# Kernel optimization log

Measured on AMD Instinct MI355X. Metric: run time of the kernel, lower is better.

## Reference

```python
import jax, jax.numpy as jnp
import numpy as np

# static config (matches init_kwargs)
C, NH, WS, H, W, NQ, PS = 384, 12, 8, 56, 56, 64, 8
HD = C // NH
SCALE = HD ** -0.5
EPS = 1e-5
MLP_H = 4 * C


def _rel_pos_index():
    ch, cw = np.meshgrid(np.arange(WS), np.arange(WS), indexing='ij')
    cf = np.stack([ch.ravel(), cw.ravel()])                      # [2, WS*WS]
    rel = cf[:, :, None] - cf[:, None, :]                        # [2, N, N]
    rel = rel.transpose(1, 2, 0)
    rel[:, :, 0] += WS - 1
    rel[:, :, 1] += WS - 1
    rel[:, :, 0] *= 2 * WS - 1
    return jnp.asarray(rel.sum(-1))                              # [N, N] int

REL_IDX = _rel_pos_index()


def _ln(x, g, b):
    mu = x.mean(-1, keepdims=True)
    var = ((x - mu) ** 2).mean(-1, keepdims=True)
    return (x - mu) * jax.lax.rsqrt(var + EPS) * g + b


def setup_inputs() -> dict:
    key = jax.random.key(0)
    ks = jax.random.split(key, 24)
    B = 16
    n = lambda k, shp, s=0.02: jax.random.normal(k, shp, dtype=jnp.float32) * s
    inp = {
        'x': jax.random.normal(ks[0], (B, H * W, C), dtype=jnp.float32),
        'query_tokens': n(ks[1], (1, NQ, C)),
        'kproj_w': n(ks[2], (C, C)), 'kproj_b': jnp.zeros((C,)),
        'kbn_g': jnp.ones((C,)), 'kbn_b': jnp.zeros((C,)),
        'vproj_w': n(ks[3], (C, C)), 'vproj_b': jnp.zeros((C,)),
        'vbn_g': jnp.ones((C,)), 'vbn_b': jnp.zeros((C,)),
        'ck_w': n(ks[4], (C, C)), 'ck_b': jnp.zeros((C,)),
        'cv_w': n(ks[5], (C, C)), 'cv_b': jnp.zeros((C,)),
        'qkv_w': n(ks[6], (C, 3 * C)), 'qkv_b': jnp.zeros((3 * C,)),
        'proj_w': n(ks[7], (C, C)), 'proj_b': jnp.zeros((C,)),
        'rpb_table': n(ks[8], ((2 * WS - 1) ** 2, NH)),
        'norm1_g': jnp.ones((C,)), 'norm1_b': jnp.zeros((C,)),
        'norm2_g': jnp.ones((C,)), 'norm2_b': jnp.zeros((C,)),
        'fc1_w': n(ks[9], (C, MLP_H)), 'fc1_b': jnp.zeros((MLP_H,)),
        'fc2_w': n(ks[10], (MLP_H, C)), 'fc2_b': jnp.zeros((C,)),
    }
    return inp


def _forward(x, query_tokens, kproj_w, kproj_b, kbn_g, kbn_b, vproj_w, vproj_b,
             vbn_g, vbn_b, ck_w, ck_b, cv_w, cv_b, qkv_w, qkv_b, proj_w, proj_b,
             rpb_table, norm1_g, norm1_b, norm2_g, norm2_b, fc1_w, fc1_b, fc2_w, fc2_b):
    B, L, _ = x.shape
    shortcut = x
    xn = _ln(x, norm1_g, norm1_b)                                # [B, L, C]

    # ---- global cross attention (pooled tokens -> learnable queries) ----
    x4 = xn.reshape(B, H, W, C)
    pooled = x4.reshape(B, H // PS, PS, W // PS, PS, C).mean(axis=(2, 4))  # [B,7,7,C]
    pooled = pooled.reshape(B, (H // PS) * (W // PS), C)         # [B, 49, C]
    # conv1x1 + BatchNorm2d (eval mode, default running stats mean=0, var=1)
    bn_scale = 1.0 / jnp.sqrt(1.0 + EPS)
    key = ((pooled @ kproj_w + kproj_b) * bn_scale) * kbn_g + kbn_b
    val = ((pooled @ vproj_w + vproj_b) * bn_scale) * vbn_g + vbn_b

    q = jnp.broadcast_to(query_tokens, (B, NQ, C))
    qh = q.reshape(B, NQ, NH, HD).transpose(0, 2, 1, 3)          # [B,NH,NQ,HD]
    kh = key.reshape(B, -1, NH, HD).transpose(0, 2, 1, 3)
    vh = val.reshape(B, -1, NH, HD).transpose(0, 2, 1, 3)
    attn = jax.nn.softmax(jnp.einsum('bhqd,bhkd->bhqk', qh, kh) * SCALE, axis=-1)
    o = jnp.einsum('bhqk,bhkd->bhqd', attn, vh).transpose(0, 2, 1, 3).reshape(B, NQ, C)
    gk = (o + q) @ ck_w + ck_b                                   # [B, NQ, C]
    gv = (o + q) @ cv_w + cv_b

    # ---- windowed attention with global kv concat ----
    nW = (H // WS) * (W // WS)
    N = WS * WS
    xw = (x4.reshape(B, H // WS, WS, W // WS, WS, C)
             .transpose(0, 1, 3, 2, 4, 5)
             .reshape(B * nW, N, C))                             # [B_, N, C]
    qkv = (xw @ qkv_w + qkv_b).reshape(B * nW, N, 3, NH, HD).transpose(2, 0, 3, 1, 4)
    wq, wk, wv = qkv[0], qkv[1], qkv[2]                          # [B_, NH, N, HD]

    gkh = jnp.broadcast_to(gk.reshape(B, 1, NQ, NH, HD), (B, nW, NQ, NH, HD))
    gkh = gkh.reshape(B * nW, NQ, NH, HD).transpose(0, 2, 1, 3)  # [B_, NH, NQ, HD]
    gvh = jnp.broadcast_to(gv.reshape(B, 1, NQ, NH, HD), (B, nW, NQ, NH, HD))
    gvh = gvh.reshape(B * nW, NQ, NH, HD).transpose(0, 2, 1, 3)
    wk = jnp.concatenate([wk, gkh], axis=2)                      # [B_, NH, N+NQ, HD]
    wv = jnp.concatenate([wv, gvh], axis=2)

    logits = jnp.einsum('bhqd,bhkd->bhqk', wq * SCALE, wk)       # [B_, NH, N, N+NQ]
    rpb = rpb_table[REL_IDX.reshape(-1)].reshape(N, N, NH).transpose(2, 0, 1)  # [NH,N,N]
    logits = logits.at[:, :, :, :N].add(rpb[None])
    wattn = jax.nn.softmax(logits, axis=-1)
    ow = jnp.einsum('bhqk,bhkd->bhqd', wattn, wv).transpose(0, 2, 1, 3).reshape(B * nW, N, C)
    ow = ow @ proj_w + proj_b

    # window reverse
    xr = (ow.reshape(B, H // WS, W // WS, WS, WS, C)
             .transpose(0, 1, 3, 2, 4, 5)
             .reshape(B, H * W, C))

    x = shortcut + xr
    h = jax.nn.gelu(_ln(x, norm2_g, norm2_b) @ fc1_w + fc1_b, approximate=False)
    return x + (h @ fc2_w + fc2_b)


def reference(x, query_tokens, kproj_w, kproj_b, kbn_g, kbn_b, vproj_w, vproj_b,
              vbn_g, vbn_b, ck_w, ck_b, cv_w, cv_b, qkv_w, qkv_b, proj_w, proj_b,
              rpb_table, norm1_g, norm1_b, norm2_g, norm2_b, fc1_w, fc1_b, fc2_w, fc2_b):
    return _forward(x, query_tokens, kproj_w, kproj_b, kbn_g, kbn_b, vproj_w, vproj_b,
                    vbn_g, vbn_b, ck_w, ck_b, cv_w, cv_b, qkv_w, qkv_b, proj_w, proj_b,
                    rpb_table, norm1_g, norm1_b, norm2_g, norm2_b, fc1_w, fc1_b, fc2_w, fc2_b)
```

## Files before the change

### kernel.cpp

```cpp
#include <hip/hip_runtime.h>
#include <math.h>

typedef __attribute__((ext_vector_type(8))) __bf16 bf16x8;
typedef __attribute__((ext_vector_type(4))) float f32x4;
typedef __attribute__((ext_vector_type(8))) unsigned short u16x8;

#define DI __device__ __forceinline__

DI float b2f(unsigned short u) { return __uint_as_float(((unsigned int)u) << 16); }
DI unsigned short f2b(float f) {
    unsigned int x = __float_as_uint(f);
    x += 0x7fffu + ((x >> 16) & 1u);
    return (unsigned short)(x >> 16);
}
DI unsigned short f2b_fast(float f) {
    __bf16 h = (__bf16)f;
    return *(unsigned short*)&h;
}

DI void gl16(const unsigned short* g, unsigned short* l) {
    __builtin_amdgcn_global_load_lds(
        (const __attribute__((address_space(1))) void*)g,
        (__attribute__((address_space(3))) void*)l,
        16, 0, 0);
}

DI float gelu_f(float v) {
    float u = v * (0.7978845608f + 0.0356774081f * v * v);
    u = fminf(fmaxf(u, -15.f), 15.f);
    float e = __expf(2.f * u);
    float th = (e - 1.f) / (e + 1.f);
    return 0.5f * v * (1.f + th);
}

#define SCALE_ATT 0.17677669529663687f
#define BN_SCALE  0.9999950000374997f

__global__ __launch_bounds__(256) void cvt_t_kernel(const float* __restrict__ in,
                                                    unsigned short* __restrict__ out,
                                                    int Kd, int Nd) {
    int i = blockIdx.x * 256 + threadIdx.x;
    if (i < Kd * Nd) {
        int k = i / Nd, n = i % Nd;
        out[(size_t)n * Kd + k] = f2b(in[i]);
    }
}

__global__ __launch_bounds__(64) void ln_kernel(const float* __restrict__ xin,
                                                const float* __restrict__ g,
                                                const float* __restrict__ bsh,
                                                unsigned short* __restrict__ out) {
    int row = blockIdx.x;
    int t = threadIdx.x;
    size_t base = (size_t)row * 384;
    float v[6];
    float s = 0.f;
#pragma unroll
    for (int p = 0; p < 6; ++p) { v[p] = xin[base + t + 64 * p]; s += v[p]; }
#pragma unroll
    for (int off = 32; off > 0; off >>= 1) s += __shfl_xor(s, off);
    float mu = s * (1.f / 384.f);
    float q = 0.f;
#pragma unroll
    for (int p = 0; p < 6; ++p) { float d = v[p] - mu; q += d * d; }
#pragma unroll
    for (int off = 32; off > 0; off >>= 1) q += __shfl_xor(q, off);
    float rstd = rsqrtf(q * (1.f / 384.f) + 1e-5f);
#pragma unroll
    for (int p = 0; p < 6; ++p) {
        int c = t + 64 * p;
        out[base + c] = f2b((v[p] - mu) * rstd * g[c] + bsh[c]);
    }
}

__global__ __launch_bounds__(384) void pool_kernel(const unsigned short* __restrict__ xn,
                                                   float* __restrict__ pooled) {
    int blk = blockIdx.x;
    int b = blk / 49, pp = blk % 49;
    int ph = pp / 7, pw = pp % 7;
    int c = threadIdx.x;
    float s = 0.f;
    for (int i = 0; i < 8; ++i) {
        size_t rb = ((size_t)b * 3136 + (size_t)(ph * 8 + i) * 56 + pw * 8) * 384;
        for (int j = 0; j < 8; ++j) s += b2f(xn[rb + (size_t)j * 384 + c]);
    }
    pooled[(size_t)blk * 384 + c] = s * (1.f / 64.f);
}

__global__ __launch_bounds__(128) void kvproj_kernel(
    const float* __restrict__ pooled,
    const float* __restrict__ kw, const float* __restrict__ kb,
    const float* __restrict__ kg, const float* __restrict__ kbb,
    const float* __restrict__ vw, const float* __restrict__ vb,
    const float* __restrict__ vg, const float* __restrict__ vbb,
    float* __restrict__ keyo, float* __restrict__ valo) {
    __shared__ float row[384];
    int r = blockIdx.x;
    int t = threadIdx.x;
    for (int c = t; c < 384; c += 128) row[c] = pooled[(size_t)r * 384 + c];
    __syncthreads();
#pragma unroll
    for (int p = 0; p < 3; ++p) {
        int c = t + 128 * p;
        float aK = 0.f, aV = 0.f;
        for (int k = 0; k < 384; ++k) {
            float rv = row[k];
            aK += rv * kw[(size_t)k * 384 + c];
            aV += rv * vw[(size_t)k * 384 + c];
        }
        keyo[(size_t)r * 384 + c] = (aK + kb[c]) * BN_SCALE * kg[c] + kbb[c];
        valo[(size_t)r * 384 + c] = (aV + vb[c]) * BN_SCALE * vg[c] + vbb[c];
    }
}

__global__ __launch_bounds__(64) void rpb_expand_kernel(const float* __restrict__ rpbt,
                                                        float* __restrict__ rpb_mat) {
    int h = blockIdx.x >> 6, q = blockIdx.x & 63;
    int k = threadIdx.x;
    int i1 = q >> 3, j1 = q & 7, i2 = k >> 3, j2 = k & 7;
    rpb_mat[((size_t)h * 64 + q) * 64 + k] = rpbt[(size_t)((i1 - i2 + 7) * 15 + (j1 - j2 + 7)) * 12 + h];
}

__global__ __launch_bounds__(64) void cross_attn_kernel(const float* __restrict__ keyg,
                                                        const float* __restrict__ valg,
                                                        const float* __restrict__ qtok,
                                                        float* __restrict__ o) {
    int b = blockIdx.x / 12, h = blockIdx.x % 12;
    __shared__ float kk[49][32];
    __shared__ float vv[49][32];
    int t = threadIdx.x;
    for (int idx = t; idx < 49 * 32; idx += 64) {
        int k = idx >> 5, d = idx & 31;
        size_t gidx = ((size_t)b * 49 + k) * 384 + h * 32 + d;
        kk[k][d] = keyg[gidx];
        vv[k][d] = valg[gidx];
    }
    __syncthreads();
    float q[32];
#pragma unroll
    for (int d = 0; d < 32; ++d) q[d] = qtok[(size_t)t * 384 + h * 32 + d] * SCALE_ATT;
    float lg[49];
    float mx = -1e30f;
#pragma unroll
    for (int k = 0; k < 49; ++k) {
        float s = 0.f;
#pragma unroll
        for (int d = 0; d < 32; ++d) s += q[d] * kk[k][d];
        lg[k] = s;
        mx = fmaxf(mx, s);
    }
    float sum = 0.f;
#pragma unroll
    for (int k = 0; k < 49; ++k) { float e = expf(lg[k] - mx); lg[k] = e; sum += e; }
    float inv = 1.f / sum;
    float od[32];
#pragma unroll
    for (int d = 0; d < 32; ++d) od[d] = 0.f;
#pragma unroll
    for (int k = 0; k < 49; ++k) {
        float wgt = lg[k];
#pragma unroll
        for (int d = 0; d < 32; ++d) od[d] += wgt * vv[k][d];
    }
#pragma unroll
    for (int d = 0; d < 32; ++d) o[((size_t)b * 64 + t) * 384 + h * 32 + d] = od[d] * inv;
}

__global__ __launch_bounds__(128) void gkv_kernel(
    const float* __restrict__ o, const float* __restrict__ qtok,
    const float* __restrict__ ckw, const float* __restrict__ ckb,
    const float* __restrict__ cvw, const float* __restrict__ cvb,
    unsigned short* __restrict__ gk, unsigned short* __restrict__ gv) {
    __shared__ float row[384];
    int r = blockIdx.x;
    int n = r & 63;
    int t = threadIdx.x;
    for (int c = t; c < 384; c += 128)
        row[c] = o[(size_t)r * 384 + c] + qtok[(size_t)n * 384 + c];
    __syncthreads();
#pragma unroll
    for (int p = 0; p < 3; ++p) {
        int c = t + 128 * p;
        float aK = 0.f, aV = 0.f;
        for (int k = 0; k < 384; ++k) {
            float rv = row[k];
            aK += rv * ckw[(size_t)k * 384 + c];
            aV += rv * cvw[(size_t)k * 384 + c];
        }
        gk[(size_t)r * 384 + c] = f2b(aK + ckb[c]);
        gv[(size_t)r * 384 + c] = f2b(aV + cvb[c]);
    }
}

template <int MODE>
__global__ __launch_bounds__(256) void gemm128(const unsigned short* __restrict__ A,
                                               const unsigned short* __restrict__ BT,
                                               const float* __restrict__ bias,
                                               int N, int K,
                                               void* __restrict__ outp,
                                               const void* __restrict__ aux0) {
    __shared__ __align__(16) unsigned short As[2][128 * 32];
    __shared__ __align__(16) unsigned short Bs[2][128 * 32];

    int nwg = gridDim.x * gridDim.y;
    int flat = blockIdx.y * gridDim.x + blockIdx.x;
    int flat2 = (flat & 7) * (nwg >> 3) + (flat >> 3);
    int bn = flat2 % gridDim.x, bm = flat2 / gridDim.x;

    int t = threadIdx.x;
    int w = t >> 6, lane = t & 63;
    int wm = w >> 1, wn = w & 1;
    int lo = lane & 15, g = lane >> 4;

    f32x4 acc[4][4];
#pragma unroll
    for (int i = 0; i < 4; ++i)
#pragma unroll
        for (int j = 0; j < 4; ++j) acc[i][j] = f32x4{0.f, 0.f, 0.f, 0.f};

    int srow = w * 32 + (lane >> 2);
    int schunk = (lane & 3) << 3;
    const unsigned short* Ap0 = A + (size_t)(bm * 128 + srow) * K + schunk;
    const unsigned short* Ap1 = A + (size_t)(bm * 128 + srow + 16) * K + schunk;
    const unsigned short* Bp0 = BT + (size_t)(bn * 128 + srow) * K + schunk;
    const unsigned short* Bp1 = BT + (size_t)(bn * 128 + srow + 16) * K + schunk;
    int d0 = (w * 32) * 32, d1 = (w * 32 + 16) * 32;

#define STAGE(buf, kb)                    \
    do {                                  \
        gl16(Ap0 + (kb), As[buf] + d0);   \
        gl16(Ap1 + (kb), As[buf] + d1);   \
        gl16(Bp0 + (kb), Bs[buf] + d0);   \
        gl16(Bp1 + (kb), Bs[buf] + d1);   \
    } while (0)

#define WAITBAR()                                          \
    do {                                                   \
        asm volatile("s_waitcnt vmcnt(0)" ::: "memory");   \
        __builtin_amdgcn_s_barrier();                      \
    } while (0)

#define COMPUTE(buf)                                                                     \
    do {                                                                                 \
        bf16x8 af[4], bfv[4];                                                            \
        _Pragma("unroll")                                                                \
        for (int m = 0; m < 4; ++m)                                                      \
            af[m] = *(const bf16x8*)(As[buf] + (wm * 64 + m * 16 + lo) * 32 + g * 8);    \
        _Pragma("unroll")                                                                \
        for (int n = 0; n < 4; ++n)                                                      \
            bfv[n] = *(const bf16x8*)(Bs[buf] + (wn * 64 + n * 16 + lo) * 32 + g * 8);   \
        _Pragma("unroll")                                                                \
        for (int m = 0; m < 4; ++m)                                                      \
            _Pragma("unroll")                                                            \
            for (int n = 0; n < 4; ++n)                                                  \
                acc[m][n] = __builtin_amdgcn_mfma_f32_16x16x32_bf16(af[m], bfv[n],       \
                                                                    acc[m][n], 0, 0, 0); \
    } while (0)

    STAGE(0, 0);
    WAITBAR();

    int nt = K >> 5;
    for (int tt = 0; tt < nt; tt += 2) {
        STAGE(1, (tt + 1) * 32);
        COMPUTE(0);
        WAITBAR();
        if (tt + 2 < nt) {
            STAGE(0, (tt + 2) * 32);
            COMPUTE(1);
            WAITBAR();
        } else {
            COMPUTE(1);
        }
    }
#undef STAGE
#undef WAITBAR
#undef COMPUTE

    int r0 = bm * 128 + wm * 64 + g * 4;
    int c0 = bn * 128 + wn * 64 + lo;
#pragma unroll
    for (int m = 0; m < 4; ++m)
#pragma unroll
        for (int n = 0; n < 4; ++n)
#pragma unroll
            for (int j = 0; j < 4; ++j) {
                int r = r0 + m * 16 + j;
                int c = c0 + n * 16;
                float v = acc[m][n][j] + bias[c];
                if (MODE == 0) {
                    ((unsigned short*)outp)[(size_t)r * N + c] = f2b(v);
                } else if (MODE == 1) {
                    int wg = r >> 6, nn = r & 63;
                    int b = wg / 49, win = wg % 49;
                    int wh = win / 7, ww = win % 7;
                    int l = ((wh << 3) + (nn >> 3)) * 56 + (ww << 3) + (nn & 7);
                    size_t idx = ((size_t)b * 3136 + l) * 384 + c;
                    ((float*)outp)[idx] = ((const float*)aux0)[idx] + v;
                } else if (MODE == 2) {
                    ((unsigned short*)outp)[(size_t)r * N + c] = f2b(gelu_f(v));
                } else {
                    float res = ((const float*)aux0)[(size_t)r * 384 + c];
                    ((float*)outp)[(size_t)r * N + c] = v + res;
                }
            }
}

__global__ __launch_bounds__(64, 2) void win_attn_mfma(const unsigned short* __restrict__ qkv,
                                                       const unsigned short* __restrict__ gkb,
                                                       const unsigned short* __restrict__ gvb,
                                                       const float* __restrict__ rpb_mat,
                                                       unsigned short* __restrict__ ow) {
    int blk = blockIdx.x;
    int wg = blk / 12, h = blk % 12;
    int b = wg / 49, win = wg % 49;
    int wh = win / 7, ww = win % 7;
    int lane = threadIdx.x;
    int lo = lane & 15, g = lane >> 4;

    __shared__ __align__(16) unsigned short VT[32 * 136];
    __shared__ __align__(16) unsigned short PL[64 * 40];

    size_t qkvbase = (size_t)b * 3136 * 1152;
    int lbase = ((wh << 3)) * 56 + (ww << 3);

    {
        int n = lane;
        int l = lbase + (n >> 3) * 56 + (n & 7);
        const unsigned short* vp = qkv + qkvbase + (size_t)l * 1152 + 768 + h * 32;
        u16x8 v0 = *(const u16x8*)(vp);
        u16x8 v1 = *(const u16x8*)(vp + 8);
        u16x8 v2 = *(const u16x8*)(vp + 16);
        u16x8 v3 = *(const u16x8*)(vp + 24);
#pragma unroll
        for (int j = 0; j < 8; ++j) {
            VT[(0 + j) * 136 + n]  = v0[j];
            VT[(8 + j) * 136 + n]  = v1[j];
            VT[(16 + j) * 136 + n] = v2[j];
            VT[(24 + j) * 136 + n] = v3[j];
        }
        const unsigned short* gp = gvb + ((size_t)b * 64 + n) * 384 + h * 32;
        v0 = *(const u16x8*)(gp);
        v1 = *(const u16x8*)(gp + 8);
        v2 = *(const u16x8*)(gp + 16);
        v3 = *(const u16x8*)(gp + 24);
#pragma unroll
        for (int j = 0; j < 8; ++j) {
            VT[(0 + j) * 136 + 64 + n]  = v0[j];
            VT[(8 + j) * 136 + 64 + n]  = v1[j];
            VT[(16 + j) * 136 + 64 + n] = v2[j];
            VT[(24 + j) * 136 + 64 + n] = v3[j];
        }
    }

    bf16x8 qf[4];
#pragma unroll
    for (int qt = 0; qt < 4; ++qt) {
        int n = qt * 16 + lo;
        int l = lbase + (n >> 3) * 56 + (n & 7);
        qf[qt] = *(const bf16x8*)(qkv + qkvbase + (size_t)l * 1152 + h * 32 + g * 8);
    }

    f32x4 S[4][8];
#pragma unroll
    for (int qt = 0; qt < 4; ++qt)
#pragma unroll
        for (int t = 0; t < 8; ++t) S[qt][t] = f32x4{0.f, 0.f, 0.f, 0.f};

#pragma unroll
    for (int t = 0; t < 8; ++t) {
        bf16x8 kf;
        if (t < 4) {
            int key = t * 16 + lo;
            int l = lbase + (key >> 3) * 56 + (key & 7);
            kf = *(const bf16x8*)(qkv + qkvbase + (size_t)l * 1152 + 384 + h * 32 + g * 8);
        } else {
            int gkey = (t - 4) * 16 + lo;
            kf = *(const bf16x8*)(gkb + ((size_t)b * 64 + gkey) * 384 + h * 32 + g * 8);
        }
#pragma unroll
        for (int qt = 0; qt < 4; ++qt)
            S[qt][t] = __builtin_amdgcn_mfma_f32_16x16x32_bf16(qf[qt], kf, S[qt][t], 0, 0, 0);
    }

    const float* rb_h = rpb_mat + (size_t)h * 4096;
    float mx[4][4];
#pragma unroll
    for (int qt = 0; qt < 4; ++qt)
#pragma unroll
        for (int j = 0; j < 4; ++j) mx[qt][j] = -1e30f;

#pragma unroll
    for (int qt = 0; qt < 4; ++qt) {
#pragma unroll
        for (int t = 0; t < 8; ++t) {
#pragma unroll
            for (int j = 0; j < 4; ++j) {
                float v = S[qt][t][j] * SCALE_ATT;
                if (t < 4) v += rb_h[(qt * 16 + g * 4 + j) * 64 + t * 16 + lo];
                S[qt][t][j] = v;
                mx[qt][j] = fmaxf(mx[qt][j], v);
            }
        }
    }
#pragma unroll
    for (int qt = 0; qt < 4; ++qt)
#pragma unroll
        for (int j = 0; j < 4; ++j) {
#pragma unroll
            for (int m = 1; m <= 8; m <<= 1)
                mx[qt][j] = fmaxf(mx[qt][j], __shfl_xor(mx[qt][j], m));
        }

    float sm[4][4];
#pragma unroll
    for (int qt = 0; qt < 4; ++qt)
#pragma unroll
        for (int j = 0; j < 4; ++j) sm[qt][j] = 0.f;
#pragma unroll
    for (int qt = 0; qt < 4; ++qt)
#pragma unroll
        for (int t = 0; t < 8; ++t)
#pragma unroll
            for (int j = 0; j < 4; ++j) {
                float p = __expf(S[qt][t][j] - mx[qt][j]);
                S[qt][t][j] = p;
                sm[qt][j] += p;
            }
#pragma unroll
    for (int qt = 0; qt < 4; ++qt)
#pragma unroll
        for (int j = 0; j < 4; ++j) {
#pragma unroll
            for (int m = 1; m <= 8; m <<= 1)
                sm[qt][j] += __shfl_xor(sm[qt][j], m);
        }
    float inv[4][4];
#pragma unroll
    for (int qt = 0; qt < 4; ++qt)
#pragma unroll
        for (int j = 0; j < 4; ++j) inv[qt][j] = 1.f / sm[qt][j];

    f32x4 O[4][2];
#pragma unroll
    for (int qt = 0; qt < 4; ++qt)
#pragma unroll
        for (int dt = 0; dt < 2; ++dt) O[qt][dt] = f32x4{0.f, 0.f, 0.f, 0.f};

#pragma unroll
    for (int c = 0; c < 4; ++c) {
        __syncthreads();
#pragma unroll
        for (int qt = 0; qt < 4; ++qt) {
            int qb = qt * 16 + g * 4;
#pragma unroll
            for (int half = 0; half < 2; ++half) {
                int t = 2 * c + half;
#pragma unroll
                for (int j = 0; j < 4; ++j)
                    PL[(qb + j) * 40 + half * 16 + lo] = f2b_fast(S[qt][t][j]);
            }
        }
        __syncthreads();
#pragma unroll
        for (int qt = 0; qt < 4; ++qt) {
            bf16x8 pa = *(const bf16x8*)(PL + (qt * 16 + lo) * 40 + g * 8);
#pragma unroll
            for (int dt = 0; dt < 2; ++dt) {
                bf16x8 vb = *(const bf16x8*)(VT + (dt * 16 + lo) * 136 + c * 32 + g * 8);
                O[qt][dt] = __builtin_amdgcn_mfma_f32_16x16x32_bf16(pa, vb, O[qt][dt], 0, 0, 0);
            }
        }
    }

#pragma unroll
    for (int qt = 0; qt < 4; ++qt)
#pragma unroll
        for (int dt = 0; dt < 2; ++dt)
#pragma unroll
            for (int j = 0; j < 4; ++j) {
                int q = qt * 16 + g * 4 + j;
                int d = dt * 16 + lo;
                ow[((size_t)wg * 64 + q) * 384 + h * 32 + d] = f2b_fast(O[qt][dt][j] * inv[qt][j]);
            }
}

static const size_t OFF_XN   = 0;
static const size_t OFF_QKV  = 38535168;
static const size_t OFF_OW   = 154140672;
static const size_t OFF_X2   = 192675840;
static const size_t OFF_PL   = 269746176;
static const size_t OFF_KEY  = 270950400;
static const size_t OFF_VAL  = 272154624;
static const size_t OFF_O    = 273358848;
static const size_t OFF_GK   = 274931712;
static const size_t OFF_GV   = 276504576;
static const size_t OFF_QKVW = 278077440;
static const size_t OFF_PRJW = 278962176;
static const size_t OFF_FC1W = 279257088;
static const size_t OFF_FC2W = 280436736;

extern "C" void kernel_launch(void* const* d_in, const int* in_sizes, int n_in,
                              void* d_out, int out_size, void* d_ws, size_t ws_size,
                              hipStream_t stream) {
    const float* x      = (const float*)d_in[0];
    const float* qtok   = (const float*)d_in[1];
    const float* kprojw = (const float*)d_in[2];
    const float* kprojb = (const float*)d_in[3];
    const float* kbng   = (const float*)d_in[4];
    const float* kbnb   = (const float*)d_in[5];
    const float* vprojw = (const float*)d_in[6];
    const float* vprojb = (const float*)d_in[7];
    const float* vbng   = (const float*)d_in[8];
    const float* vbnb   = (const float*)d_in[9];
    const float* ckw    = (const float*)d_in[10];
    const float* ckb    = (const float*)d_in[11];
    const float* cvw    = (const float*)d_in[12];
    const float* cvb    = (const float*)d_in[13];
    const float* qkvw   = (const float*)d_in[14];
    const float* qkvb   = (const float*)d_in[15];
    const float* projw  = (const float*)d_in[16];
    const float* projb  = (const float*)d_in[17];
    const float* rpbt   = (const float*)d_in[18];
    const float* n1g    = (const float*)d_in[19];
    const float* n1b    = (const float*)d_in[20];
    const float* n2g    = (const float*)d_in[21];
    const float* n2b    = (const float*)d_in[22];
    const float* fc1w   = (const float*)d_in[23];
    const float* fc1b   = (const float*)d_in[24];
    const float* fc2w   = (const float*)d_in[25];
    const float* fc2b   = (const float*)d_in[26];

    char* wsb = (char*)d_ws;
    unsigned short* xn     = (unsigned short*)(wsb + OFF_XN);
    unsigned short* qkvbf  = (unsigned short*)(wsb + OFF_QKV);
    unsigned short* owbf   = (unsigned short*)(wsb + OFF_OW);
    float* x2      = (float*)(wsb + OFF_X2);
    float* pooled  = (float*)(wsb + OFF_PL);
    float* rpb_mat = (float*)(wsb + OFF_PL);
    float* keyg    = (float*)(wsb + OFF_KEY);
    float* valg    = (float*)(wsb + OFF_VAL);
    float* obuf    = (float*)(wsb + OFF_O);
    unsigned short* gkb = (unsigned short*)(wsb + OFF_GK);
    unsigned short* gvb = (unsigned short*)(wsb + OFF_GV);
    unsigned short* qkvw_t = (unsigned short*)(wsb + OFF_QKVW);
    unsigned short* prjw_t = (unsigned short*)(wsb + OFF_PRJW);
    unsigned short* fc1w_t = (unsigned short*)(wsb + OFF_FC1W);
    unsigned short* fc2w_t = (unsigned short*)(wsb + OFF_FC2W);
    unsigned short* ln2out = (unsigned short*)(wsb + OFF_XN);
    unsigned short* hbuf   = (unsigned short*)(wsb + OFF_QKV);

    cvt_t_kernel<<<(442368 + 255) / 256, 256, 0, stream>>>(qkvw, qkvw_t, 384, 1152);
    cvt_t_kernel<<<(147456 + 255) / 256, 256, 0, stream>>>(projw, prjw_t, 384, 384);
    cvt_t_kernel<<<(589824 + 255) / 256, 256, 0, stream>>>(fc1w, fc1w_t, 384, 1536);
    cvt_t_kernel<<<(589824 + 255) / 256, 256, 0, stream>>>(fc2w, fc2w_t, 1536, 384);
    ln_kernel<<<50176, 64, 0, stream>>>(x, n1g, n1b, xn);
    pool_kernel<<<784, 384, 0, stream>>>(xn, pooled);
    kvproj_kernel<<<784, 128, 0, stream>>>(pooled, kprojw, kprojb, kbng, kbnb,
                                           vprojw, vprojb, vbng, vbnb, keyg, valg);
    rpb_expand_kernel<<<768, 64, 0, stream>>>(rpbt, rpb_mat);
    cross_attn_kernel<<<192, 64, 0, stream>>>(keyg, valg, qtok, obuf);
    gkv_kernel<<<1024, 128, 0, stream>>>(obuf, qtok, ckw, ckb, cvw, cvb, gkb, gvb);
    gemm128<0><<<dim3(9, 392), 256, 0, stream>>>(xn, qkvw_t, qkvb, 1152, 384, qkvbf, nullptr);
    win_attn_mfma<<<9408, 64, 0, stream>>>(qkvbf, gkb, gvb, rpb_mat, owbf);
    gemm128<1><<<dim3(3, 392), 256, 0, stream>>>(owbf, prjw_t, projb, 384, 384, x2, x);
    ln_kernel<<<50176, 64, 0, stream>>>(x2, n2g, n2b, ln2out);
    gemm128<2><<<dim3(12, 392), 256, 0, stream>>>(ln2out, fc1w_t, fc1b, 1536, 384, hbuf, nullptr);
    gemm128<3><<<dim3(3, 392), 256, 0, stream>>>(hbuf, fc2w_t, fc2b, 384, 1536, (float*)d_out, x2);
}
```

Baseline: 823.3 us.

## Triple-buffer GEMM LDS staging with partial vmcnt waits

The bf16 MFMA GEMM goes from double-buffered to triple-buffered LDS tiles. Each stage now waits with vmcnt(4), so one tile's global-to-LDS loads stay in flight while the current tile is computed, and it uses a single barrier per k-step instead of a full drain. The aim is to hide global load latency better. In exchange, shared memory per block rises to 48KB, and the launch bound now asks for 3 blocks per SM, which may put pressure on registers or LDS. The loop unrolls by 3, so it assumes K/32 is a multiple of 3, which holds for the 384 and 1536 K sizes used.

Measured after the change: 715.6 us. 13.1% less time.

```diff
diff --git a/kernel.cpp b/kernel.cpp
--- a/kernel.cpp
+++ b/kernel.cpp
@@ -193,14 +193,14 @@
 }
 
 template <int MODE>
-__global__ __launch_bounds__(256) void gemm128(const unsigned short* __restrict__ A,
-                                               const unsigned short* __restrict__ BT,
-                                               const float* __restrict__ bias,
-                                               int N, int K,
-                                               void* __restrict__ outp,
-                                               const void* __restrict__ aux0) {
-    __shared__ __align__(16) unsigned short As[2][128 * 32];
-    __shared__ __align__(16) unsigned short Bs[2][128 * 32];
+__global__ __launch_bounds__(256, 3) void gemm128(const unsigned short* __restrict__ A,
+                                                  const unsigned short* __restrict__ BT,
+                                                  const float* __restrict__ bias,
+                                                  int N, int K,
+                                                  void* __restrict__ outp,
+                                                  const void* __restrict__ aux0) {
+    __shared__ __align__(16) unsigned short As[3][128 * 32];
+    __shared__ __align__(16) unsigned short Bs[3][128 * 32];
 
     int nwg = gridDim.x * gridDim.y;
     int flat = blockIdx.y * gridDim.x + blockIdx.x;
@@ -234,11 +234,8 @@
         gl16(Bp1 + (kb), Bs[buf] + d1);   \
     } while (0)
 
-#define WAITBAR()                                          \
-    do {                                                   \
-        asm volatile("s_waitcnt vmcnt(0)" ::: "memory");   \
-        __builtin_amdgcn_s_barrier();                      \
-    } while (0)
+#define WAIT4() asm volatile("s_waitcnt vmcnt(4)" ::: "memory")
+#define WAIT0() asm volatile("s_waitcnt vmcnt(0)" ::: "memory")
 
 #define COMPUTE(buf)                                                                     \
     do {                                                                                 \
@@ -258,23 +255,26 @@
     } while (0)
 
     STAGE(0, 0);
-    WAITBAR();
+    STAGE(1, 32);
 
     int nt = K >> 5;
-    for (int tt = 0; tt < nt; tt += 2) {
-        STAGE(1, (tt + 1) * 32);
+    for (int tt = 0; tt < nt; tt += 3) {
+        if (tt + 1 < nt) WAIT4(); else WAIT0();
+        __builtin_amdgcn_s_barrier();
+        if (tt + 2 < nt) STAGE(2, (tt + 2) * 32);
         COMPUTE(0);
-        WAITBAR();
-        if (tt + 2 < nt) {
-            STAGE(0, (tt + 2) * 32);
-            COMPUTE(1);
-            WAITBAR();
-        } else {
-            COMPUTE(1);
-        }
+        if (tt + 2 < nt) WAIT4(); else WAIT0();
+        __builtin_amdgcn_s_barrier();
+        if (tt + 3 < nt) STAGE(0, (tt + 3) * 32);
+        COMPUTE(1);
+        if (tt + 3 < nt) WAIT4(); else WAIT0();
+        __builtin_amdgcn_s_barrier();
+        if (tt + 4 < nt) STAGE(1, (tt + 4) * 32);
+        COMPUTE(2);
     }
 #undef STAGE
-#undef WAITBAR
+#undef WAIT4
+#undef WAIT0
 #undef COMPUTE
 
     int r0 = bm * 128 + wm * 64 + g * 4;
```

## Double GEMM K-tile to 64 with XOR-swizzled LDS and split staging

Applied to the files above, without the earlier changes.

The bf16 MFMA GEMM now stages 64-wide K tiles instead of 32-wide ones, halving the number of barrier rounds per output tile. LDS rows are stored with an XOR swizzle to avoid bank conflicts on the fragment reads. Loads for the next A and B tiles are issued separately and interleaved between the two compute halves of the current tile to overlap memory with MFMA work. Launch bounds now request 2 blocks per SIMD. The cost is doubled LDS use per block, which may limit occupancy, and the unrolled loop assumes K/64 is even.

New measurement: 752.6 us. -8.6%, faster.

```diff
diff --git a/kernel.cpp b/kernel.cpp
--- a/kernel.cpp
+++ b/kernel.cpp
@@ -193,14 +193,14 @@
 }
 
 template <int MODE>
-__global__ __launch_bounds__(256) void gemm128(const unsigned short* __restrict__ A,
-                                               const unsigned short* __restrict__ BT,
-                                               const float* __restrict__ bias,
-                                               int N, int K,
-                                               void* __restrict__ outp,
-                                               const void* __restrict__ aux0) {
-    __shared__ __align__(16) unsigned short As[2][128 * 32];
-    __shared__ __align__(16) unsigned short Bs[2][128 * 32];
+__global__ __launch_bounds__(256, 2) void gemm128(const unsigned short* __restrict__ A,
+                                                  const unsigned short* __restrict__ BT,
+                                                  const float* __restrict__ bias,
+                                                  int N, int K,
+                                                  void* __restrict__ outp,
+                                                  const void* __restrict__ aux0) {
+    __shared__ __align__(16) unsigned short As[2][128 * 64];
+    __shared__ __align__(16) unsigned short Bs[2][128 * 64];
 
     int nwg = gridDim.x * gridDim.y;
     int flat = blockIdx.y * gridDim.x + blockIdx.x;
@@ -218,20 +218,29 @@
 #pragma unroll
         for (int j = 0; j < 4; ++j) acc[i][j] = f32x4{0.f, 0.f, 0.f, 0.f};
 
-    int srow = w * 32 + (lane >> 2);
-    int schunk = (lane & 3) << 3;
-    const unsigned short* Ap0 = A + (size_t)(bm * 128 + srow) * K + schunk;
-    const unsigned short* Ap1 = A + (size_t)(bm * 128 + srow + 16) * K + schunk;
-    const unsigned short* Bp0 = BT + (size_t)(bn * 128 + srow) * K + schunk;
-    const unsigned short* Bp1 = BT + (size_t)(bn * 128 + srow + 16) * K + schunk;
-    int d0 = (w * 32) * 32, d1 = (w * 32 + 16) * 32;
-
-#define STAGE(buf, kb)                    \
-    do {                                  \
-        gl16(Ap0 + (kb), As[buf] + d0);   \
-        gl16(Ap1 + (kb), As[buf] + d1);   \
-        gl16(Bp0 + (kb), Bs[buf] + d0);   \
-        gl16(Bp1 + (kb), Bs[buf] + d1);   \
+    int arow = w * 32 + (lane >> 3);
+    int acol = (((lane & 7) ^ (lane >> 3)) << 3);
+    const unsigned short* ApB = A + (size_t)(bm * 128 + arow) * K + acol;
+    const unsigned short* BpB = BT + (size_t)(bn * 128 + arow) * K + acol;
+    int sK8 = 8 * K;
+
+    int gx0 = (((0 + g) ^ (lo & 7)) << 3);
+    int gx1 = (((4 + g) ^ (lo & 7)) << 3);
+
+#define STAGE_A(buf, kb)                                              \
+    do {                                                              \
+        gl16(ApB + (kb),            As[buf] + (w * 32 + 0) * 64);     \
+        gl16(ApB + (kb) + sK8,      As[buf] + (w * 32 + 8) * 64);     \
+        gl16(ApB + (kb) + 2 * sK8,  As[buf] + (w * 32 + 16) * 64);    \
+        gl16(ApB + (kb) + 3 * sK8,  As[buf] + (w * 32 + 24) * 64);    \
+    } while (0)
+
+#define STAGE_B(buf, kb)                                              \
+    do {                                                              \
+        gl16(BpB + (kb),            Bs[buf] + (w * 32 + 0) * 64);     \
+        gl16(BpB + (kb) + sK8,      Bs[buf] + (w * 32 + 8) * 64);     \
+        gl16(BpB + (kb) + 2 * sK8,  Bs[buf] + (w * 32 + 16) * 64);    \
+        gl16(BpB + (kb) + 3 * sK8,  Bs[buf] + (w * 32 + 24) * 64);    \
     } while (0)
 
 #define WAITBAR()                                          \
@@ -240,42 +249,43 @@
         __builtin_amdgcn_s_barrier();                      \
     } while (0)
 
-#define COMPUTE(buf)                                                                     \
-    do {                                                                                 \
-        bf16x8 af[4], bfv[4];                                                            \
-        _Pragma("unroll")                                                                \
-        for (int m = 0; m < 4; ++m)                                                      \
-            af[m] = *(const bf16x8*)(As[buf] + (wm * 64 + m * 16 + lo) * 32 + g * 8);    \
-        _Pragma("unroll")                                                                \
-        for (int n = 0; n < 4; ++n)                                                      \
-            bfv[n] = *(const bf16x8*)(Bs[buf] + (wn * 64 + n * 16 + lo) * 32 + g * 8);   \
-        _Pragma("unroll")                                                                \
-        for (int m = 0; m < 4; ++m)                                                      \
-            _Pragma("unroll")                                                            \
-            for (int n = 0; n < 4; ++n)                                                  \
-                acc[m][n] = __builtin_amdgcn_mfma_f32_16x16x32_bf16(af[m], bfv[n],       \
-                                                                    acc[m][n], 0, 0, 0); \
+#define COMPUTE_HALF(buf, gxk)                                                            \
+    do {                                                                                  \
+        bf16x8 af[4], bfv[4];                                                             \
+        _Pragma("unroll")                                                                 \
+        for (int m = 0; m < 4; ++m)                                                       \
+            af[m] = *(const bf16x8*)(As[buf] + (wm * 64 + m * 16 + lo) * 64 + (gxk));     \
+        _Pragma("unroll")                                                                 \
+        for (int n = 0; n < 4; ++n)                                                       \
+            bfv[n] = *(const bf16x8*)(Bs[buf] + (wn * 64 + n * 16 + lo) * 64 + (gxk));    \
+        _Pragma("unroll")                                                                 \
+        for (int m = 0; m < 4; ++m)                                                       \
+            _Pragma("unroll")                                                             \
+            for (int n = 0; n < 4; ++n)                                                   \
+                acc[m][n] = __builtin_amdgcn_mfma_f32_16x16x32_bf16(af[m], bfv[n],        \
+                                                                    acc[m][n], 0, 0, 0);  \
     } while (0)
 
-    STAGE(0, 0);
-    WAITBAR();
-
-    int nt = K >> 5;
+    STAGE_A(0, 0);
+    STAGE_B(0, 0);
+
+    int nt = K >> 6;
     for (int tt = 0; tt < nt; tt += 2) {
-        STAGE(1, (tt + 1) * 32);
-        COMPUTE(0);
         WAITBAR();
-        if (tt + 2 < nt) {
-            STAGE(0, (tt + 2) * 32);
-            COMPUTE(1);
-            WAITBAR();
-        } else {
-            COMPUTE(1);
-        }
-    }
-#undef STAGE
+        if (tt + 1 < nt) STAGE_A(1, (tt + 1) * 64);
+        COMPUTE_HALF(0, gx0);
+        if (tt + 1 < nt) STAGE_B(1, (tt + 1) * 64);
+        COMPUTE_HALF(0, gx1);
+        WAITBAR();
+        if (tt + 2 < nt) STAGE_A(0, (tt + 2) * 64);
+        COMPUTE_HALF(1, gx0);
+        if (tt + 2 < nt) STAGE_B(0, (tt + 2) * 64);
+        COMPUTE_HALF(1, gx1);
+    }
+#undef STAGE_A
+#undef STAGE_B
 #undef WAITBAR
-#undef COMPUTE
+#undef COMPUTE_HALF
 
     int r0 = bm * 128 + wm * 64 + g * 4;
     int c0 = bn * 128 + wn * 64 + lo;
```
